# Kernel tuning notes

Measured on AMD Instinct MI355X. Metric: run time of the kernel, lower is better.

The kernel has to match this reference:

```python
import jax, jax.numpy as jnp
import numpy as np

H = 1024

def _gru_layer(x_seq, W_ih, W_hh, b_ih, b_hh):
    # x_seq: [B, T, in]; W_ih: [3H, in]; W_hh: [3H, H]
    B = x_seq.shape[0]
    gx = jnp.einsum('bti,gi->btg', x_seq, W_ih) + b_ih  # [B, T, 3H] input gates precomputed

    def step(h, gx_t):
        gh = h @ W_hh.T + b_hh  # [B, 3H]
        xr, xz, xn = jnp.split(gx_t, 3, axis=-1)
        hr, hz, hn = jnp.split(gh, 3, axis=-1)
        r = jax.nn.sigmoid(xr + hr)
        z = jax.nn.sigmoid(xz + hz)
        n = jnp.tanh(xn + r * hn)
        h_new = (1.0 - z) * n + z * h
        return h_new, h_new

    h0 = jnp.zeros((B, W_hh.shape[1]), dtype=x_seq.dtype)
    _, out = jax.lax.scan(step, h0, jnp.swapaxes(gx, 0, 1))  # scan over T
    return jnp.swapaxes(out, 0, 1)  # [B, T, H]

def setup_inputs() -> dict:
    key = jax.random.key(0)
    ks = jax.random.split(key, 8)
    s = 0.03  # ~1/sqrt(H) init scale to avoid gate saturation
    return {
        'tokens': jax.random.randint(ks[0], (16, 1024), 0, 32000),
        'emb': jax.random.normal(ks[1], (32000, H), jnp.float32),
        'W_ih_l0': jax.random.normal(ks[2], (3 * H, H), jnp.float32) * s,
        'W_hh_l0': jax.random.normal(ks[3], (3 * H, H), jnp.float32) * s,
        'b_ih_l0': jnp.zeros((3 * H,), jnp.float32),
        'b_hh_l0': jnp.zeros((3 * H,), jnp.float32),
        'W_ih_l1': jax.random.normal(ks[4], (3 * H, H), jnp.float32) * s,
        'W_hh_l1': jax.random.normal(ks[5], (3 * H, H), jnp.float32) * s,
        'b_ih_l1': jnp.zeros((3 * H,), jnp.float32),
        'b_hh_l1': jnp.zeros((3 * H,), jnp.float32),
        'W_lin': jax.random.normal(ks[6], (128, H), jnp.float32) * s,
        'b_lin': jnp.zeros((128,), jnp.float32),
    }

def reference(tokens, emb, W_ih_l0, W_hh_l0, b_ih_l0, b_hh_l0,
              W_ih_l1, W_hh_l1, b_ih_l1, b_hh_l1, W_lin, b_lin):
    x = emb[tokens]  # [B, T, H]
    h1 = _gru_layer(x, W_ih_l0, W_hh_l0, b_ih_l0, b_hh_l0)
    h2 = _gru_layer(h1, W_ih_l1, W_hh_l1, b_ih_l1, b_hh_l1)
    logits = jnp.einsum('bth,ch->btc', h2, W_lin) + b_lin  # [B, T, C]
    # F.log_softmax with no dim on a 3D tensor uses dim=1 (PyTorch deprecated default)
    return jax.nn.log_softmax(logits, axis=1)
```

## Files before the change

kernel.cpp:

```cpp
#include <hip/hip_runtime.h>
#include <stdint.h>

typedef unsigned short u16;
typedef __attribute__((ext_vector_type(8))) short short8;
typedef __attribute__((ext_vector_type(4))) float f32x4;

#define T_SEQ 1024
#define HDIM  1024
#define NG    3072
#define SLOT  16384
#define FSTRIDE 32

__device__ __forceinline__ u16 f2bf(float f) {
  unsigned u = __float_as_uint(f);
  u += 0x7FFF + ((u >> 16) & 1);
  return (u16)(u >> 16);
}
__device__ __forceinline__ float bf2f(u16 h) {
  return __uint_as_float(((unsigned)h) << 16);
}

__device__ __forceinline__ void gld16(void* lds, const void* g) {
  __builtin_amdgcn_global_load_lds(
      (const __attribute__((address_space(1))) unsigned*)g,
      (__attribute__((address_space(3))) unsigned*)lds, 16, 0, 0);
}

__device__ __forceinline__ void st_agent_u32(unsigned* p, unsigned v) {
  __hip_atomic_store(p, v, __ATOMIC_RELAXED, __HIP_MEMORY_SCOPE_AGENT);
}
__device__ __forceinline__ unsigned ld_agent_u32(const unsigned* p) {
  return __hip_atomic_load(p, __ATOMIC_RELAXED, __HIP_MEMORY_SCOPE_AGENT);
}

__device__ __forceinline__ void poll16(const unsigned* flags, int wave, int lane, unsigned need) {
  if (lane < 16) {
    const unsigned* f = flags + (size_t)(16 * wave + lane) * FSTRIDE;
    while (ld_agent_u32(f) < need) {}
  }
  asm volatile("" ::: "memory");
}

__global__ void cast5_kernel(const float* __restrict__ s0, const float* __restrict__ s1,
                             const float* __restrict__ s2, const float* __restrict__ s3,
                             const float* __restrict__ s4,
                             u16* __restrict__ d0, u16* __restrict__ d1,
                             u16* __restrict__ d2, u16* __restrict__ d3,
                             u16* __restrict__ d4, unsigned* __restrict__ flags) {
  if (blockIdx.x == 0) {
#pragma unroll
    for (int k = 0; k < 32; ++k) flags[threadIdx.x * 32 + k] = 0;
  }
  int bid = blockIdx.x;
  const float* s; u16* d; size_t base;
  if (bid < 3072)       { s = s0; d = d0; base = (size_t)bid * 1024; }
  else if (bid < 6144)  { s = s1; d = d1; base = (size_t)(bid - 3072) * 1024; }
  else if (bid < 9216)  { s = s2; d = d2; base = (size_t)(bid - 6144) * 1024; }
  else if (bid < 12288) { s = s3; d = d3; base = (size_t)(bid - 9216) * 1024; }
  else                  { s = s4; d = d4; base = (size_t)(bid - 12288) * 1024; }
  size_t i = base + (size_t)threadIdx.x * 4;
  float4 v = *(const float4*)(s + i);
  unsigned lo = (unsigned)f2bf(v.x) | ((unsigned)f2bf(v.y) << 16);
  unsigned hi = (unsigned)f2bf(v.z) | ((unsigned)f2bf(v.w) << 16);
  uint2 o; o.x = lo; o.y = hi;
  *(uint2*)(d + i) = o;
}

__global__ void gather_cast_kernel(const int* __restrict__ tokens,
                                   const float* __restrict__ emb,
                                   u16* __restrict__ xbf) {
  int row = blockIdx.x;
  int tok = tokens[row];
  const float4* src = (const float4*)(emb + (size_t)tok * HDIM);
  float4 v = src[threadIdx.x];
  unsigned lo = (unsigned)f2bf(v.x) | ((unsigned)f2bf(v.y) << 16);
  unsigned hi = (unsigned)f2bf(v.z) | ((unsigned)f2bf(v.w) << 16);
  uint2 o; o.x = lo; o.y = hi;
  *(uint2*)(xbf + (size_t)row * HDIM + (size_t)threadIdx.x * 4) = o;
}

template <bool OUT_BF16, bool A_PACKED, bool ADD_BIAS>
__global__ __launch_bounds__(256)
void gemm_bt(const u16* __restrict__ A, const u16* __restrict__ Bt,
             void* __restrict__ Cout, const float* __restrict__ bias,
             int M, int N) {
  const int K = 1024;
  __shared__ u16 As[128 * 32];
  __shared__ u16 Bs[128 * 32];
  const int tid = threadIdx.x;
  const int wave = tid >> 6, lane = tid & 63;
  const int quad = lane >> 4, l16 = lane & 15;
  const int wm = (wave & 1) * 64, wn = (wave >> 1) * 64;
  const int m0 = blockIdx.x * 128, n0 = blockIdx.y * 128;
  const int srow = tid >> 2, scol = (tid & 3) * 8;

  size_t abase0, abase1;
  {
    int r0 = m0 + srow, r1 = m0 + 64 + srow;
    if (A_PACKED) {
      abase0 = (size_t)((r0 & 1023) + 1) * SLOT + (size_t)(r0 >> 10) * 16 +
               (size_t)(scol & 8) + (size_t)(scol >> 4) * 256;
      abase1 = (size_t)((r1 & 1023) + 1) * SLOT + (size_t)(r1 >> 10) * 16 +
               (size_t)(scol & 8) + (size_t)(scol >> 4) * 256;
    } else {
      abase0 = (size_t)r0 * K + scol;
      abase1 = (size_t)r1 * K + scol;
    }
  }
  const size_t bbase0 = (size_t)(n0 + srow) * K + scol;
  const size_t bbase1 = (size_t)(n0 + 64 + srow) * K + scol;

  f32x4 acc[4][4] = {};

  for (int kk = 0; kk < K; kk += 32) {
    __syncthreads();
    size_t ka = A_PACKED ? (size_t)kk * 16 : (size_t)kk;
    gld16(&As[srow * 32 + scol],        A + abase0 + ka);
    gld16(&As[(64 + srow) * 32 + scol], A + abase1 + ka);
    gld16(&Bs[srow * 32 + scol],        Bt + bbase0 + kk);
    gld16(&Bs[(64 + srow) * 32 + scol], Bt + bbase1 + kk);
    __syncthreads();
    short8 af[4], bfr[4];
#pragma unroll
    for (int mt = 0; mt < 4; ++mt)
      af[mt] = *(const short8*)&As[(wm + mt * 16 + l16) * 32 + quad * 8];
#pragma unroll
    for (int nt = 0; nt < 4; ++nt)
      bfr[nt] = *(const short8*)&Bs[(wn + nt * 16 + l16) * 32 + quad * 8];
#pragma unroll
    for (int mt = 0; mt < 4; ++mt)
#pragma unroll
      for (int nt = 0; nt < 4; ++nt)
        acc[mt][nt] = __builtin_amdgcn_mfma_f32_16x16x32_bf16(af[mt], bfr[nt], acc[mt][nt], 0, 0, 0);
  }
#pragma unroll
  for (int mt = 0; mt < 4; ++mt) {
#pragma unroll
    for (int nt = 0; nt < 4; ++nt) {
#pragma unroll
      for (int r = 0; r < 4; ++r) {
        int m = m0 + wm + mt * 16 + quad * 4 + r;
        int n = n0 + wn + nt * 16 + l16;
        float v = acc[mt][nt][r];
        if (ADD_BIAS) v += bias[n];
        if (OUT_BF16) ((u16*)Cout)[(size_t)m * N + n] = f2bf(v);
        else          ((float*)Cout)[(size_t)m * N + n] = v;
      }
    }
  }
}

__global__ __launch_bounds__(256, 1)
void fused_scan_kernel(const u16* __restrict__ gx0,
                       u16* __restrict__ h1p, u16* __restrict__ h2p,
                       const u16* __restrict__ Whh0, const u16* __restrict__ Wih1,
                       const u16* __restrict__ Whh1,
                       const float* __restrict__ bih0, const float* __restrict__ bhh0,
                       const float* __restrict__ bih1, const float* __restrict__ bhh1,
                       unsigned* __restrict__ flags0, unsigned* __restrict__ flags1) {
  const int tid = threadIdx.x;
  const int wave = tid >> 6, lane = tid & 63;
  const int quad = lane >> 4, l16 = lane & 15;
  const int eb = tid >> 4, ej = tid & 15;

  __shared__ float part[4][6][256];
  __shared__ float biasS[2][3][16];

  const int fragoff = (16 * wave + (quad >> 1)) * 256 + l16 * 16 + (quad & 1) * 8;

  if (blockIdx.x < 64) {
    const int wg = blockIdx.x, j0 = wg * 16;
    short8 wf[3][8];
#pragma unroll
    for (int g = 0; g < 3; ++g)
#pragma unroll
      for (int s = 0; s < 8; ++s)
        wf[g][s] = *(const short8*)&Whh0[(size_t)(g * 1024 + j0 + l16) * 1024 + wave * 256 + s * 32 + quad * 8];
    if (tid < 96) {
      int a = tid / 48, rem = tid % 48, g = rem >> 4, jl = rem & 15;
      biasS[a][g][jl] = (a ? bhh0 : bih0)[g * 1024 + j0 + jl];
    }
    if (tid < 128) st_agent_u32((unsigned*)h1p + wg * 128 + tid, 0u);
    __syncthreads();
    if (tid == 0)
      __hip_atomic_store(flags0 + (size_t)wg * FSTRIDE, 1u, __ATOMIC_RELEASE, __HIP_MEMORY_SCOPE_AGENT);

    const u16* gxp = gx0 + (size_t)eb * T_SEQ * NG + j0 + ej;
    u16 gxu0 = gxp[0], gxu1 = gxp[1024], gxu2 = gxp[2048];
    float hprev = 0.f;

    for (int t = 0; t < T_SEQ; ++t) {
      poll16(flags0, wave, lane, (unsigned)(t + 1));
      int tn = (t + 1 < T_SEQ) ? t + 1 : t;
      const u16* gpn = gx0 + ((size_t)eb * T_SEQ + tn) * NG + j0 + ej;
      u16 ng0 = gpn[0], ng1 = gpn[1024], ng2 = gpn[2048];
      const u16* src = h1p + (size_t)t * SLOT + fragoff;
      short8 af[8];
#pragma unroll
      for (int s = 0; s < 8; ++s) af[s] = *(const short8*)(src + s * 512);
      f32x4 a0 = {0.f,0.f,0.f,0.f}, a1 = {0.f,0.f,0.f,0.f}, a2 = {0.f,0.f,0.f,0.f};
#pragma unroll
      for (int s = 0; s < 8; ++s) {
        a0 = __builtin_amdgcn_mfma_f32_16x16x32_bf16(af[s], wf[0][s], a0, 0, 0, 0);
        a1 = __builtin_amdgcn_mfma_f32_16x16x32_bf16(af[s], wf[1][s], a1, 0, 0, 0);
        a2 = __builtin_amdgcn_mfma_f32_16x16x32_bf16(af[s], wf[2][s], a2, 0, 0, 0);
      }
#pragma unroll
      for (int r = 0; r < 4; ++r) {
        int o = (quad * 4 + r) * 16 + l16;
        part[wave][0][o] = a0[r]; part[wave][1][o] = a1[r]; part[wave][2][o] = a2[r];
      }
      __syncthreads();
      float ghr = part[0][0][tid] + part[1][0][tid] + part[2][0][tid] + part[3][0][tid] + biasS[1][0][ej];
      float ghz = part[0][1][tid] + part[1][1][tid] + part[2][1][tid] + part[3][1][tid] + biasS[1][1][ej];
      float ghn = part[0][2][tid] + part[1][2][tid] + part[2][2][tid] + part[3][2][tid] + biasS[1][2][ej];
      float xr = bf2f(gxu0) + biasS[0][0][ej] + ghr;
      float xz = bf2f(gxu1) + biasS[0][1][ej] + ghz;
      float xn = bf2f(gxu2) + biasS[0][2][ej];
      float r_ = 1.f / (1.f + __expf(-xr));
      float z_ = 1.f / (1.f + __expf(-xz));
      float pre = fminf(fmaxf(xn + r_ * ghn, -15.f), 15.f);
      float e2 = __expf(2.f * pre);
      float n_ = (e2 - 1.f) / (e2 + 1.f);
      float hn = (1.f - z_) * n_ + z_ * hprev;
      hprev = hn;
      gxu0 = ng0; gxu1 = ng1; gxu2 = ng2;

      unsigned mine = (unsigned)f2bf(hn);
      unsigned other = __shfl_xor(mine, 1);
      if (!(tid & 1))
        st_agent_u32((unsigned*)h1p + (size_t)(t + 1) * (SLOT / 2) + wg * 128 + (tid >> 1),
                     mine | (other << 16));
      __syncthreads();
      if (tid == 0)
        __hip_atomic_store(flags0 + (size_t)wg * FSTRIDE, (unsigned)(t + 2), __ATOMIC_RELEASE, __HIP_MEMORY_SCOPE_AGENT);
    }
  } else {
    const int wg = blockIdx.x - 64, j0 = wg * 16;
    short8 wfX[3][8], wfH[3][8];
#pragma unroll
    for (int g = 0; g < 3; ++g)
#pragma unroll
      for (int s = 0; s < 8; ++s) {
        size_t row = (size_t)(g * 1024 + j0 + l16) * 1024 + wave * 256 + s * 32 + quad * 8;
        wfX[g][s] = *(const short8*)&Wih1[row];
        wfH[g][s] = *(const short8*)&Whh1[row];
      }
    if (tid < 96) {
      int a = tid / 48, rem = tid % 48, g = rem >> 4, jl = rem & 15;
      biasS[a][g][jl] = (a ? bhh1 : bih1)[g * 1024 + j0 + jl];
    }
    if (tid < 128) st_agent_u32((unsigned*)h2p + wg * 128 + tid, 0u);
    __syncthreads();
    if (tid == 0)
      __hip_atomic_store(flags1 + (size_t)wg * FSTRIDE, 1u, __ATOMIC_RELEASE, __HIP_MEMORY_SCOPE_AGENT);

    short8 af1[8];
    poll16(flags0, wave, lane, 2u);
    {
      const u16* s1 = h1p + (size_t)SLOT + fragoff;
#pragma unroll
      for (int s = 0; s < 8; ++s) af1[s] = *(const short8*)(s1 + s * 512);
    }
    float hprev = 0.f;

    for (int t = 0; t < T_SEQ; ++t) {
      f32x4 x0 = {0.f,0.f,0.f,0.f}, x1 = {0.f,0.f,0.f,0.f}, x2 = {0.f,0.f,0.f,0.f};
#pragma unroll
      for (int s = 0; s < 8; ++s) {
        x0 = __builtin_amdgcn_mfma_f32_16x16x32_bf16(af1[s], wfX[0][s], x0, 0, 0, 0);
        x1 = __builtin_amdgcn_mfma_f32_16x16x32_bf16(af1[s], wfX[1][s], x1, 0, 0, 0);
        x2 = __builtin_amdgcn_mfma_f32_16x16x32_bf16(af1[s], wfX[2][s], x2, 0, 0, 0);
      }
      poll16(flags1, wave, lane, (unsigned)(t + 1));
      short8 af2[8];
      const u16* s2 = h2p + (size_t)t * SLOT + fragoff;
#pragma unroll
      for (int s = 0; s < 8; ++s) af2[s] = *(const short8*)(s2 + s * 512);
      if (t + 1 < T_SEQ) {
        poll16(flags0, wave, lane, (unsigned)(t + 3));
        const u16* s1 = h1p + (size_t)(t + 2) * SLOT + fragoff;
#pragma unroll
        for (int s = 0; s < 8; ++s) af1[s] = *(const short8*)(s1 + s * 512);
      }
      f32x4 h0 = {0.f,0.f,0.f,0.f}, h1a = {0.f,0.f,0.f,0.f}, h2a = {0.f,0.f,0.f,0.f};
#pragma unroll
      for (int s = 0; s < 8; ++s) {
        h0  = __builtin_amdgcn_mfma_f32_16x16x32_bf16(af2[s], wfH[0][s], h0, 0, 0, 0);
        h1a = __builtin_amdgcn_mfma_f32_16x16x32_bf16(af2[s], wfH[1][s], h1a, 0, 0, 0);
        h2a = __builtin_amdgcn_mfma_f32_16x16x32_bf16(af2[s], wfH[2][s], h2a, 0, 0, 0);
      }
#pragma unroll
      for (int r = 0; r < 4; ++r) {
        int o = (quad * 4 + r) * 16 + l16;
        part[wave][0][o] = x0[r];  part[wave][1][o] = x1[r];  part[wave][2][o] = x2[r];
        part[wave][3][o] = h0[r];  part[wave][4][o] = h1a[r]; part[wave][5][o] = h2a[r];
      }
      __syncthreads();
      float sxr = part[0][0][tid] + part[1][0][tid] + part[2][0][tid] + part[3][0][tid] + biasS[0][0][ej];
      float sxz = part[0][1][tid] + part[1][1][tid] + part[2][1][tid] + part[3][1][tid] + biasS[0][1][ej];
      float sxn = part[0][2][tid] + part[1][2][tid] + part[2][2][tid] + part[3][2][tid] + biasS[0][2][ej];
      float shr = part[0][3][tid] + part[1][3][tid] + part[2][3][tid] + part[3][3][tid] + biasS[1][0][ej];
      float shz = part[0][4][tid] + part[1][4][tid] + part[2][4][tid] + part[3][4][tid] + biasS[1][1][ej];
      float shn = part[0][5][tid] + part[1][5][tid] + part[2][5][tid] + part[3][5][tid] + biasS[1][2][ej];
      float r_ = 1.f / (1.f + __expf(-(sxr + shr)));
      float z_ = 1.f / (1.f + __expf(-(sxz + shz)));
      float pre = fminf(fmaxf(sxn + r_ * shn, -15.f), 15.f);
      float e2 = __expf(2.f * pre);
      float n_ = (e2 - 1.f) / (e2 + 1.f);
      float hn = (1.f - z_) * n_ + z_ * hprev;
      hprev = hn;

      unsigned mine = (unsigned)f2bf(hn);
      unsigned other = __shfl_xor(mine, 1);
      if (!(tid & 1))
        st_agent_u32((unsigned*)h2p + (size_t)(t + 1) * (SLOT / 2) + wg * 128 + (tid >> 1),
                     mine | (other << 16));
      __syncthreads();
      if (tid == 0)
        __hip_atomic_store(flags1 + (size_t)wg * FSTRIDE, (unsigned)(t + 2), __ATOMIC_RELEASE, __HIP_MEMORY_SCOPE_AGENT);
    }
  }
}

__global__ void logsoftmax_kernel(float* __restrict__ out) {
  int b = blockIdx.x, cg = blockIdx.y;
  int ci = threadIdx.x & 15, ts = threadIdx.x >> 4;
  int c = cg * 16 + ci;
  float m = -1e30f, s = 0.f;
  for (int t = ts; t < T_SEQ; t += 16) {
    float v = out[((size_t)b * T_SEQ + t) * 128 + c];
    if (v > m) { s = s * __expf(m - v) + 1.f; m = v; }
    else s += __expf(v - m);
  }
  __shared__ float mS[16][16], sS[16][16];
  mS[ts][ci] = m; sS[ts][ci] = s;
  __syncthreads();
  if (ts == 0) {
    float M = mS[0][ci], S = sS[0][ci];
#pragma unroll
    for (int k = 1; k < 16; ++k) {
      float m2 = mS[k][ci], s2 = sS[k][ci];
      float nm = fmaxf(M, m2);
      S = S * __expf(M - nm) + s2 * __expf(m2 - nm);
      M = nm;
    }
    sS[0][ci] = M + logf(S);
  }
  __syncthreads();
  float lsd = sS[0][ci];
  for (int t = ts; t < T_SEQ; t += 16) {
    size_t i = ((size_t)b * T_SEQ + t) * 128 + c;
    out[i] -= lsd;
  }
}

extern "C" void kernel_launch(void* const* d_in, const int* in_sizes, int n_in,
                              void* d_out, int out_size, void* d_ws, size_t ws_size,
                              hipStream_t stream) {
  const int*   tokens = (const int*)d_in[0];
  const float* emb  = (const float*)d_in[1];
  const float* Wih0 = (const float*)d_in[2];
  const float* Whh0 = (const float*)d_in[3];
  const float* bih0 = (const float*)d_in[4];
  const float* bhh0 = (const float*)d_in[5];
  const float* Wih1 = (const float*)d_in[6];
  const float* Whh1 = (const float*)d_in[7];
  const float* bih1 = (const float*)d_in[8];
  const float* bhh1 = (const float*)d_in[9];
  const float* Wlin = (const float*)d_in[10];
  const float* blin = (const float*)d_in[11];
  float* out = (float*)d_out;

  uint8_t* ws = (uint8_t*)d_ws;
  size_t off = 0;
  auto alloc = [&](size_t bytes) -> void* {
    void* p = ws + off;
    off += (bytes + 255) & ~(size_t)255;
    return p;
  };
  u16* h1p   = (u16*)alloc((size_t)(T_SEQ + 1) * SLOT * 2);
  u16* h2p   = (u16*)alloc((size_t)(T_SEQ + 1) * SLOT * 2);
  u16* xbf   = h2p;
  u16* gxbuf = (u16*)alloc((size_t)16384 * NG * 2);
  u16* wih0b = (u16*)alloc((size_t)NG * HDIM * 2);
  u16* whh0b = (u16*)alloc((size_t)NG * HDIM * 2);
  u16* wih1b = (u16*)alloc((size_t)NG * HDIM * 2);
  u16* whh1b = (u16*)alloc((size_t)NG * HDIM * 2);
  u16* wlinb = (u16*)alloc((size_t)128 * HDIM * 2);
  unsigned* flags = (unsigned*)alloc(32768);

  cast5_kernel<<<dim3(12416), dim3(256), 0, stream>>>(
      Wih0, Whh0, Wih1, Whh1, Wlin, wih0b, whh0b, wih1b, whh1b, wlinb, flags);
  gather_cast_kernel<<<dim3(16384), dim3(256), 0, stream>>>(tokens, emb, xbf);
  gemm_bt<true, false, false><<<dim3(128, 24), dim3(256), 0, stream>>>(
      xbf, wih0b, gxbuf, nullptr, 16384, NG);
  fused_scan_kernel<<<dim3(128), dim3(256), 0, stream>>>(
      gxbuf, h1p, h2p, whh0b, wih1b, whh1b, bih0, bhh0, bih1, bhh1,
      flags, flags + 64 * FSTRIDE);
  gemm_bt<false, true, true><<<dim3(128, 1), dim3(256), 0, stream>>>(
      h2p, wlinb, out, blin, 16384, 128);
  logsoftmax_kernel<<<dim3(16, 8), dim3(256), 0, stream>>>(out);
}
```

Before: 3.883 ms.

## Replace flag polling with tagged-data handoff and ring buffer in GRU scan

Each hidden-state word is now stored as a 64-bit pair of two bf16 values plus a step tag, so consumers poll the data itself instead of a separate per-workgroup release flag. This removes the flag store, release fence and barrier from each step. Layer 0 writes into a 64-slot ring buffer and only occasionally waits on layer-1 progress counters, and layer 1's input weights move from registers to LDS. The cost is double the bytes per hidden-state transfer, a clear kernel over a larger workspace, and a reworked A-operand load in the final projection GEMM to unpack the tagged layout.

Measured after the change: 6.340 ms. 1.63x slower.

```diff
diff --git a/kernel.cpp b/kernel.cpp
--- a/kernel.cpp
+++ b/kernel.cpp
@@ -2,13 +2,16 @@
 #include <stdint.h>
 
 typedef unsigned short u16;
+typedef unsigned int u32;
+typedef unsigned long long u64;
 typedef __attribute__((ext_vector_type(8))) short short8;
 typedef __attribute__((ext_vector_type(4))) float f32x4;
 
 #define T_SEQ 1024
 #define HDIM  1024
 #define NG    3072
-#define SLOT  16384
+#define RING  64
+#define SLOTU 16384
 #define FSTRIDE 32
 
 __device__ __forceinline__ u16 f2bf(float f) {
@@ -33,12 +36,36 @@
   return __hip_atomic_load(p, __ATOMIC_RELAXED, __HIP_MEMORY_SCOPE_AGENT);
 }
 
-__device__ __forceinline__ void poll16(const unsigned* flags, int wave, int lane, unsigned need) {
-  if (lane < 16) {
-    const unsigned* f = flags + (size_t)(16 * wave + lane) * FSTRIDE;
-    while (ld_agent_u32(f) < need) {}
-  }
-  asm volatile("" ::: "memory");
+__device__ __forceinline__ void load_slot(short8 af[8], const u64* slot64,
+                                          int fb64, unsigned exptag) {
+  for (;;) {
+    unsigned bad = 0;
+#pragma unroll
+    for (int s = 0; s < 8; ++s) {
+      const u64* p = slot64 + fb64 + s * 256;
+      u64 w0 = __hip_atomic_load(p + 0, __ATOMIC_RELAXED, __HIP_MEMORY_SCOPE_AGENT);
+      u64 w1 = __hip_atomic_load(p + 1, __ATOMIC_RELAXED, __HIP_MEMORY_SCOPE_AGENT);
+      u64 w2 = __hip_atomic_load(p + 2, __ATOMIC_RELAXED, __HIP_MEMORY_SCOPE_AGENT);
+      u64 w3 = __hip_atomic_load(p + 3, __ATOMIC_RELAXED, __HIP_MEMORY_SCOPE_AGENT);
+      bad |= ((unsigned)(w0 >> 32) ^ exptag) | ((unsigned)(w1 >> 32) ^ exptag) |
+             ((unsigned)(w2 >> 32) ^ exptag) | ((unsigned)(w3 >> 32) ^ exptag);
+      uint4 q; q.x = (unsigned)w0; q.y = (unsigned)w1; q.z = (unsigned)w2; q.w = (unsigned)w3;
+      af[s] = *(const short8*)&q;
+    }
+    if (__ballot(bad == 0) == ~0ull) return;
+  }
+}
+
+__device__ __forceinline__ void store_pair(unsigned* base32, size_t idx32,
+                                           unsigned pk, unsigned tag) {
+  u64 w = (u64)pk | ((u64)tag << 32);
+  __hip_atomic_store((u64*)base32 + (idx32 >> 1), w,
+                     __ATOMIC_RELAXED, __HIP_MEMORY_SCOPE_AGENT);
+}
+
+__global__ void clear_kernel(uint4* __restrict__ p, unsigned n) {
+  unsigned i = blockIdx.x * 256 + threadIdx.x;
+  if (i < n) { uint4 z; z.x = z.y = z.z = z.w = 0u; p[i] = z; }
 }
 
 __global__ void cast5_kernel(const float* __restrict__ s0, const float* __restrict__ s1,
@@ -46,11 +73,7 @@
                              const float* __restrict__ s4,
                              u16* __restrict__ d0, u16* __restrict__ d1,
                              u16* __restrict__ d2, u16* __restrict__ d3,
-                             u16* __restrict__ d4, unsigned* __restrict__ flags) {
-  if (blockIdx.x == 0) {
-#pragma unroll
-    for (int k = 0; k < 32; ++k) flags[threadIdx.x * 32 + k] = 0;
-  }
+                             u16* __restrict__ d4) {
   int bid = blockIdx.x;
   const float* s; u16* d; size_t base;
   if (bid < 3072)       { s = s0; d = d0; base = (size_t)bid * 1024; }
@@ -79,13 +102,13 @@
   *(uint2*)(xbf + (size_t)row * HDIM + (size_t)threadIdx.x * 4) = o;
 }
 
-template <bool OUT_BF16, bool A_PACKED, bool ADD_BIAS>
+template <bool OUT_BF16, int AMODE, bool ADD_BIAS>
 __global__ __launch_bounds__(256)
 void gemm_bt(const u16* __restrict__ A, const u16* __restrict__ Bt,
              void* __restrict__ Cout, const float* __restrict__ bias,
              int M, int N) {
   const int K = 1024;
-  __shared__ u16 As[128 * 32];
+  __shared__ __align__(16) unsigned char AsRaw[16384];
   __shared__ u16 Bs[128 * 32];
   const int tid = threadIdx.x;
   const int wave = tid >> 6, lane = tid & 63;
@@ -94,18 +117,20 @@
   const int m0 = blockIdx.x * 128, n0 = blockIdx.y * 128;
   const int srow = tid >> 2, scol = (tid & 3) * 8;
 
-  size_t abase0, abase1;
-  {
-    int r0 = m0 + srow, r1 = m0 + 64 + srow;
-    if (A_PACKED) {
-      abase0 = (size_t)((r0 & 1023) + 1) * SLOT + (size_t)(r0 >> 10) * 16 +
-               (size_t)(scol & 8) + (size_t)(scol >> 4) * 256;
-      abase1 = (size_t)((r1 & 1023) + 1) * SLOT + (size_t)(r1 >> 10) * 16 +
-               (size_t)(scol & 8) + (size_t)(scol >> 4) * 256;
-    } else {
-      abase0 = (size_t)r0 * K + scol;
-      abase1 = (size_t)r1 * K + scol;
-    }
+  size_t abase0 = 0, abase1 = 0;
+  size_t abaseP[4];
+  if constexpr (AMODE == 1) {
+    int li = tid & 7;
+#pragma unroll
+    for (int rd = 0; rd < 4; ++rd) {
+      int r = m0 + rd * 32 + (tid >> 3);
+      int b = r >> 10, tt = r & 1023;
+      abaseP[rd] = (size_t)(tt + 1) * SLOTU + (size_t)b * 16 +
+                   (size_t)(li >> 2) * 256 + (size_t)(li & 3) * 4;
+    }
+  } else {
+    abase0 = (size_t)(m0 + srow) * K + scol;
+    abase1 = (size_t)(m0 + 64 + srow) * K + scol;
   }
   const size_t bbase0 = (size_t)(n0 + srow) * K + scol;
   const size_t bbase1 = (size_t)(n0 + 64 + srow) * K + scol;
@@ -114,16 +139,37 @@
 
   for (int kk = 0; kk < K; kk += 32) {
     __syncthreads();
-    size_t ka = A_PACKED ? (size_t)kk * 16 : (size_t)kk;
-    gld16(&As[srow * 32 + scol],        A + abase0 + ka);
-    gld16(&As[(64 + srow) * 32 + scol], A + abase1 + ka);
+    if constexpr (AMODE == 1) {
+      u32* As32 = (u32*)AsRaw;
+      const u32* Apk = (const u32*)A;
+#pragma unroll
+      for (int rd = 0; rd < 4; ++rd)
+        gld16(As32 + rd * 1024 + tid * 4, Apk + abaseP[rd] + (size_t)(kk >> 4) * 256);
+    } else {
+      u16* As = (u16*)AsRaw;
+      gld16(&As[srow * 32 + scol],        A + abase0 + kk);
+      gld16(&As[(64 + srow) * 32 + scol], A + abase1 + kk);
+    }
     gld16(&Bs[srow * 32 + scol],        Bt + bbase0 + kk);
     gld16(&Bs[(64 + srow) * 32 + scol], Bt + bbase1 + kk);
     __syncthreads();
     short8 af[4], bfr[4];
-#pragma unroll
-    for (int mt = 0; mt < 4; ++mt)
-      af[mt] = *(const short8*)&As[(wm + mt * 16 + l16) * 32 + quad * 8];
+    if constexpr (AMODE == 1) {
+      const u32* As32 = (const u32*)AsRaw;
+#pragma unroll
+      for (int mt = 0; mt < 4; ++mt) {
+        const uint4* q = (const uint4*)&As32[(wm + mt * 16 + l16) * 32 +
+                                             (quad >> 1) * 16 + (quad & 1) * 8];
+        uint4 q0 = q[0], q1 = q[1];
+        uint4 d; d.x = q0.x; d.y = q0.z; d.z = q1.x; d.w = q1.z;
+        af[mt] = *(const short8*)&d;
+      }
+    } else {
+      const u16* As = (const u16*)AsRaw;
+#pragma unroll
+      for (int mt = 0; mt < 4; ++mt)
+        af[mt] = *(const short8*)&As[(wm + mt * 16 + l16) * 32 + quad * 8];
+    }
 #pragma unroll
     for (int nt = 0; nt < 4; ++nt)
       bfr[nt] = *(const short8*)&Bs[(wn + nt * 16 + l16) * 32 + quad * 8];
@@ -152,12 +198,12 @@
 
 __global__ __launch_bounds__(256, 1)
 void fused_scan_kernel(const u16* __restrict__ gx0,
-                       u16* __restrict__ h1p, u16* __restrict__ h2p,
+                       unsigned* __restrict__ h1p, unsigned* __restrict__ h2p,
                        const u16* __restrict__ Whh0, const u16* __restrict__ Wih1,
                        const u16* __restrict__ Whh1,
                        const float* __restrict__ bih0, const float* __restrict__ bhh0,
                        const float* __restrict__ bih1, const float* __restrict__ bhh1,
-                       unsigned* __restrict__ flags0, unsigned* __restrict__ flags1) {
+                       unsigned* __restrict__ prog) {
   const int tid = threadIdx.x;
   const int wave = tid >> 6, lane = tid & 63;
   const int quad = lane >> 4, l16 = lane & 15;
@@ -165,8 +211,9 @@
 
   __shared__ float part[4][6][256];
   __shared__ float biasS[2][3][16];
-
-  const int fragoff = (16 * wave + (quad >> 1)) * 256 + l16 * 16 + (quad & 1) * 8;
+  __shared__ u16 wx[4 * 3 * 8 * 4 * 16 * 8];
+
+  const int fb64 = (((16 * wave + (quad >> 1)) * 256 + l16 * 16 + (quad & 1) * 8) >> 1);
 
   if (blockIdx.x < 64) {
     const int wg = blockIdx.x, j0 = wg * 16;
@@ -180,24 +227,19 @@
       int a = tid / 48, rem = tid % 48, g = rem >> 4, jl = rem & 15;
       biasS[a][g][jl] = (a ? bhh0 : bih0)[g * 1024 + j0 + jl];
     }
-    if (tid < 128) st_agent_u32((unsigned*)h1p + wg * 128 + tid, 0u);
-    __syncthreads();
-    if (tid == 0)
-      __hip_atomic_store(flags0 + (size_t)wg * FSTRIDE, 1u, __ATOMIC_RELEASE, __HIP_MEMORY_SCOPE_AGENT);
-
     const u16* gxp = gx0 + (size_t)eb * T_SEQ * NG + j0 + ej;
     u16 gxu0 = gxp[0], gxu1 = gxp[1024], gxu2 = gxp[2048];
     float hprev = 0.f;
+    unsigned vfgen = 64;
 
     for (int t = 0; t < T_SEQ; ++t) {
-      poll16(flags0, wave, lane, (unsigned)(t + 1));
       int tn = (t + 1 < T_SEQ) ? t + 1 : t;
       const u16* gpn = gx0 + ((size_t)eb * T_SEQ + tn) * NG + j0 + ej;
       u16 ng0 = gpn[0], ng1 = gpn[1024], ng2 = gpn[2048];
-      const u16* src = h1p + (size_t)t * SLOT + fragoff;
+
       short8 af[8];
-#pragma unroll
-      for (int s = 0; s < 8; ++s) af[s] = *(const short8*)(src + s * 512);
+      load_slot(af, (const u64*)h1p + (size_t)(t & (RING - 1)) * (SLOTU / 2), fb64, (unsigned)t);
+
       f32x4 a0 = {0.f,0.f,0.f,0.f}, a1 = {0.f,0.f,0.f,0.f}, a2 = {0.f,0.f,0.f,0.f};
 #pragma unroll
       for (int s = 0; s < 8; ++s) {
@@ -226,63 +268,60 @@
       hprev = hn;
       gxu0 = ng0; gxu1 = ng1; gxu2 = ng2;
 
+      if ((unsigned)(t + 1) > vfgen) {
+        unsigned thr = (unsigned)(t - 32);
+        for (;;) {
+          unsigned v = 0xFFFFFFFFu;
+          if (lane < 16) v = ld_agent_u32(prog + (size_t)(16 * wave + lane) * FSTRIDE);
+          if (__ballot(v >= thr) == ~0ull) break;
+        }
+        vfgen = thr + 65;
+      }
+
       unsigned mine = (unsigned)f2bf(hn);
       unsigned other = __shfl_xor(mine, 1);
       if (!(tid & 1))
-        st_agent_u32((unsigned*)h1p + (size_t)(t + 1) * (SLOT / 2) + wg * 128 + (tid >> 1),
-                     mine | (other << 16));
+        store_pair(h1p, (size_t)((t + 1) & (RING - 1)) * SLOTU + wg * 256 + eb * 16 + ej,
+                   mine | (other << 16), (unsigned)(t + 1));
       __syncthreads();
-      if (tid == 0)
-        __hip_atomic_store(flags0 + (size_t)wg * FSTRIDE, (unsigned)(t + 2), __ATOMIC_RELEASE, __HIP_MEMORY_SCOPE_AGENT);
     }
   } else {
     const int wg = blockIdx.x - 64, j0 = wg * 16;
-    short8 wfX[3][8], wfH[3][8];
+    short8 wfH[3][8];
 #pragma unroll
     for (int g = 0; g < 3; ++g)
 #pragma unroll
       for (int s = 0; s < 8; ++s) {
         size_t row = (size_t)(g * 1024 + j0 + l16) * 1024 + wave * 256 + s * 32 + quad * 8;
-        wfX[g][s] = *(const short8*)&Wih1[row];
         wfH[g][s] = *(const short8*)&Whh1[row];
+        short8 wv = *(const short8*)&Wih1[row];
+        *(short8*)&wx[((((wave * 3 + g) * 8 + s) * 4 + quad) * 16 + l16) * 8] = wv;
       }
     if (tid < 96) {
       int a = tid / 48, rem = tid % 48, g = rem >> 4, jl = rem & 15;
       biasS[a][g][jl] = (a ? bhh1 : bih1)[g * 1024 + j0 + jl];
     }
-    if (tid < 128) st_agent_u32((unsigned*)h2p + wg * 128 + tid, 0u);
-    __syncthreads();
-    if (tid == 0)
-      __hip_atomic_store(flags1 + (size_t)wg * FSTRIDE, 1u, __ATOMIC_RELEASE, __HIP_MEMORY_SCOPE_AGENT);
-
+    float hprev = 0.f;
     short8 af1[8];
-    poll16(flags0, wave, lane, 2u);
-    {
-      const u16* s1 = h1p + (size_t)SLOT + fragoff;
-#pragma unroll
-      for (int s = 0; s < 8; ++s) af1[s] = *(const short8*)(s1 + s * 512);
-    }
-    float hprev = 0.f;
+    load_slot(af1, (const u64*)h1p + (size_t)1 * (SLOTU / 2), fb64, 1u);
 
     for (int t = 0; t < T_SEQ; ++t) {
       f32x4 x0 = {0.f,0.f,0.f,0.f}, x1 = {0.f,0.f,0.f,0.f}, x2 = {0.f,0.f,0.f,0.f};
 #pragma unroll
       for (int s = 0; s < 8; ++s) {
-        x0 = __builtin_amdgcn_mfma_f32_16x16x32_bf16(af1[s], wfX[0][s], x0, 0, 0, 0);
-        x1 = __builtin_amdgcn_mfma_f32_16x16x32_bf16(af1[s], wfX[1][s], x1, 0, 0, 0);
-        x2 = __builtin_amdgcn_mfma_f32_16x16x32_bf16(af1[s], wfX[2][s], x2, 0, 0, 0);
-      }
-      poll16(flags1, wave, lane, (unsigned)(t + 1));
+        short8 w0 = *(const short8*)&wx[((((wave * 3 + 0) * 8 + s) * 4 + quad) * 16 + l16) * 8];
+        short8 w1 = *(const short8*)&wx[((((wave * 3 + 1) * 8 + s) * 4 + quad) * 16 + l16) * 8];
+        short8 w2 = *(const short8*)&wx[((((wave * 3 + 2) * 8 + s) * 4 + quad) * 16 + l16) * 8];
+        x0 = __builtin_amdgcn_mfma_f32_16x16x32_bf16(af1[s], w0, x0, 0, 0, 0);
+        x1 = __builtin_amdgcn_mfma_f32_16x16x32_bf16(af1[s], w1, x1, 0, 0, 0);
+        x2 = __builtin_amdgcn_mfma_f32_16x16x32_bf16(af1[s], w2, x2, 0, 0, 0);
+      }
       short8 af2[8];
-      const u16* s2 = h2p + (size_t)t * SLOT + fragoff;
-#pragma unroll
-      for (int s = 0; s < 8; ++s) af2[s] = *(const short8*)(s2 + s * 512);
-      if (t + 1 < T_SEQ) {
-        poll16(flags0, wave, lane, (unsigned)(t + 3));
-        const u16* s1 = h1p + (size_t)(t + 2) * SLOT + fragoff;
-#pragma unroll
-        for (int s = 0; s < 8; ++s) af1[s] = *(const short8*)(s1 + s * 512);
-      }
+      load_slot(af2, (const u64*)h2p + (size_t)t * (SLOTU / 2), fb64, (unsigned)t);
+      if (t + 1 < T_SEQ)
+        load_slot(af1, (const u64*)h1p + (size_t)((t + 2) & (RING - 1)) * (SLOTU / 2), fb64,
+                  (unsigned)(t + 2));
+
       f32x4 h0 = {0.f,0.f,0.f,0.f}, h1a = {0.f,0.f,0.f,0.f}, h2a = {0.f,0.f,0.f,0.f};
 #pragma unroll
       for (int s = 0; s < 8; ++s) {
@@ -314,11 +353,11 @@
       unsigned mine = (unsigned)f2bf(hn);
       unsigned other = __shfl_xor(mine, 1);
       if (!(tid & 1))
-        st_agent_u32((unsigned*)h2p + (size_t)(t + 1) * (SLOT / 2) + wg * 128 + (tid >> 1),
-                     mine | (other << 16));
+        store_pair(h2p, (size_t)(t + 1) * SLOTU + wg * 256 + eb * 16 + ej,
+                   mine | (other << 16), (unsigned)(t + 1));
       __syncthreads();
       if (tid == 0)
-        __hip_atomic_store(flags1 + (size_t)wg * FSTRIDE, (unsigned)(t + 2), __ATOMIC_RELEASE, __HIP_MEMORY_SCOPE_AGENT);
+        st_agent_u32(prog + (size_t)wg * FSTRIDE, (unsigned)(t + 1));
     }
   }
 }
@@ -379,26 +418,29 @@
     off += (bytes + 255) & ~(size_t)255;
     return p;
   };
-  u16* h1p   = (u16*)alloc((size_t)(T_SEQ + 1) * SLOT * 2);
-  u16* h2p   = (u16*)alloc((size_t)(T_SEQ + 1) * SLOT * 2);
-  u16* xbf   = h2p;
+  unsigned* h1p  = (unsigned*)alloc((size_t)RING * SLOTU * 4);
+  unsigned* h2p  = (unsigned*)alloc((size_t)(T_SEQ + 1) * SLOTU * 4);
+  unsigned* prog = (unsigned*)alloc((size_t)64 * FSTRIDE * 4);
+  size_t clearBytes = (size_t)RING * SLOTU * 4 + (size_t)(T_SEQ + 1) * SLOTU * 4 +
+                      (size_t)64 * FSTRIDE * 4;
+  u16* xbf   = (u16*)h2p;
   u16* gxbuf = (u16*)alloc((size_t)16384 * NG * 2);
   u16* wih0b = (u16*)alloc((size_t)NG * HDIM * 2);
   u16* whh0b = (u16*)alloc((size_t)NG * HDIM * 2);
   u16* wih1b = (u16*)alloc((size_t)NG * HDIM * 2);
   u16* whh1b = (u16*)alloc((size_t)NG * HDIM * 2);
   u16* wlinb = (u16*)alloc((size_t)128 * HDIM * 2);
-  unsigned* flags = (unsigned*)alloc(32768);
 
   cast5_kernel<<<dim3(12416), dim3(256), 0, stream>>>(
-      Wih0, Whh0, Wih1, Whh1, Wlin, wih0b, whh0b, wih1b, whh1b, wlinb, flags);
+      Wih0, Whh0, Wih1, Whh1, Wlin, wih0b, whh0b, wih1b, whh1b, wlinb);
   gather_cast_kernel<<<dim3(16384), dim3(256), 0, stream>>>(tokens, emb, xbf);
-  gemm_bt<true, false, false><<<dim3(128, 24), dim3(256), 0, stream>>>(
+  gemm_bt<true, 0, false><<<dim3(128, 24), dim3(256), 0, stream>>>(
       xbf, wih0b, gxbuf, nullptr, 16384, NG);
+  unsigned n16 = (unsigned)(clearBytes / 16);
+  clear_kernel<<<dim3((n16 + 255) / 256), dim3(256), 0, stream>>>((uint4*)h1p, n16);
   fused_scan_kernel<<<dim3(128), dim3(256), 0, stream>>>(
-      gxbuf, h1p, h2p, whh0b, wih1b, whh1b, bih0, bhh0, bih1, bhh1,
-      flags, flags + 64 * FSTRIDE);
-  gemm_bt<false, true, true><<<dim3(128, 1), dim3(256), 0, stream>>>(
-      h2p, wlinb, out, blin, 16384, 128);
+      gxbuf, h1p, h2p, whh0b, wih1b, whh1b, bih0, bhh0, bih1, bhh1, prog);
+  gemm_bt<false, 1, true><<<dim3(128, 1), dim3(256), 0, stream>>>(
+      (const u16*)h2p, wlinb, out, blin, 16384, 128);
   logsoftmax_kernel<<<dim3(16, 8), dim3(256), 0, stream>>>(out);
 }
```

## Use per-wave flags, double-buffered partials, LDS-resident Wih1, and timestep-major gx layout

Applied to the files above, without the earlier changes.

The scan kernel now publishes progress per wave instead of per block. Each wave waits for its own stores to complete and sets its own flag, which removes the two block-wide barriers per step, and consumers poll 64 flags per wave. The partial-sum LDS buffer is double-buffered so the single remaining barrier per step is enough. The layer-1 Wih1 fragments move from registers to LDS to relieve register pressure, and the gx GEMM writes its output in a timestep-major layout so each step reads gx contiguously. The risks are more polling traffic across 64 lanes, extra LDS reads per step, and flag ordering that relies on s_waitcnt instead of release atomics.

Result: faster. 3.263 ms (-16.0%).

```diff
diff --git a/kernel.cpp b/kernel.cpp
--- a/kernel.cpp
+++ b/kernel.cpp
@@ -2,6 +2,7 @@
 #include <stdint.h>
 
 typedef unsigned short u16;
+typedef unsigned int u32;
 typedef __attribute__((ext_vector_type(8))) short short8;
 typedef __attribute__((ext_vector_type(4))) float f32x4;
 
@@ -33,11 +34,9 @@
   return __hip_atomic_load(p, __ATOMIC_RELAXED, __HIP_MEMORY_SCOPE_AGENT);
 }
 
-__device__ __forceinline__ void poll16(const unsigned* flags, int wave, int lane, unsigned need) {
-  if (lane < 16) {
-    const unsigned* f = flags + (size_t)(16 * wave + lane) * FSTRIDE;
-    while (ld_agent_u32(f) < need) {}
-  }
+__device__ __forceinline__ void poll64(const unsigned* flags, int wave, int lane, unsigned need) {
+  const unsigned* f = flags + (size_t)(64 * wave + lane) * FSTRIDE;
+  while (ld_agent_u32(f) < need) {}
   asm volatile("" ::: "memory");
 }
 
@@ -49,7 +48,7 @@
                              u16* __restrict__ d4, unsigned* __restrict__ flags) {
   if (blockIdx.x == 0) {
 #pragma unroll
-    for (int k = 0; k < 32; ++k) flags[threadIdx.x * 32 + k] = 0;
+    for (int k = 0; k < 64; ++k) flags[threadIdx.x * 64 + k] = 0;
   }
   int bid = blockIdx.x;
   const float* s; u16* d; size_t base;
@@ -79,7 +78,7 @@
   *(uint2*)(xbf + (size_t)row * HDIM + (size_t)threadIdx.x * 4) = o;
 }
 
-template <bool OUT_BF16, bool A_PACKED, bool ADD_BIAS>
+template <int OUT_MODE, bool A_PACKED, bool ADD_BIAS>
 __global__ __launch_bounds__(256)
 void gemm_bt(const u16* __restrict__ A, const u16* __restrict__ Bt,
              void* __restrict__ Cout, const float* __restrict__ bias,
@@ -143,8 +142,13 @@
         int n = n0 + wn + nt * 16 + l16;
         float v = acc[mt][nt][r];
         if (ADD_BIAS) v += bias[n];
-        if (OUT_BF16) ((u16*)Cout)[(size_t)m * N + n] = f2bf(v);
-        else          ((float*)Cout)[(size_t)m * N + n] = v;
+        if (OUT_MODE == 2) {
+          int t = m & 1023, b = m >> 10, g = n >> 10, c = n & 1023;
+          size_t idx = ((((size_t)t * 64 + (c >> 4)) * 3 + g) * 16 + b) * 16 + (c & 15);
+          ((u16*)Cout)[idx] = f2bf(v);
+        } else {
+          ((float*)Cout)[(size_t)m * N + n] = v;
+        }
       }
     }
   }
@@ -152,7 +156,7 @@
 
 __global__ __launch_bounds__(256, 1)
 void fused_scan_kernel(const u16* __restrict__ gx0,
-                       u16* __restrict__ h1p, u16* __restrict__ h2p,
+                       u16* __restrict__ h1seq, u16* __restrict__ h2seq,
                        const u16* __restrict__ Whh0, const u16* __restrict__ Wih1,
                        const u16* __restrict__ Whh1,
                        const float* __restrict__ bih0, const float* __restrict__ bhh0,
@@ -163,8 +167,9 @@
   const int quad = lane >> 4, l16 = lane & 15;
   const int eb = tid >> 4, ej = tid & 15;
 
-  __shared__ float part[4][6][256];
+  __shared__ float part[2][4][6][256];
   __shared__ float biasS[2][3][16];
+  __shared__ u16 wx[4 * 3 * 8 * 4 * 16 * 8];
 
   const int fragoff = (16 * wave + (quad >> 1)) * 256 + l16 * 16 + (quad & 1) * 8;
 
@@ -180,21 +185,18 @@
       int a = tid / 48, rem = tid % 48, g = rem >> 4, jl = rem & 15;
       biasS[a][g][jl] = (a ? bhh0 : bih0)[g * 1024 + j0 + jl];
     }
-    if (tid < 128) st_agent_u32((unsigned*)h1p + wg * 128 + tid, 0u);
-    __syncthreads();
-    if (tid == 0)
-      __hip_atomic_store(flags0 + (size_t)wg * FSTRIDE, 1u, __ATOMIC_RELEASE, __HIP_MEMORY_SCOPE_AGENT);
-
-    const u16* gxp = gx0 + (size_t)eb * T_SEQ * NG + j0 + ej;
-    u16 gxu0 = gxp[0], gxu1 = gxp[1024], gxu2 = gxp[2048];
+    if (lane < 32) st_agent_u32((unsigned*)h1seq + wg * 128 + wave * 32 + lane, 0u);
+    asm volatile("s_waitcnt vmcnt(0)" ::: "memory");
+    if (lane == 0) st_agent_u32(flags0 + (size_t)(wg * 4 + wave) * FSTRIDE, 1u);
+
+    const u16* gxp = gx0 + (size_t)(wg * 3) * 256 + eb * 16 + ej;
+    u16 gxu0 = gxp[0], gxu1 = gxp[256], gxu2 = gxp[512];
     float hprev = 0.f;
 
     for (int t = 0; t < T_SEQ; ++t) {
-      poll16(flags0, wave, lane, (unsigned)(t + 1));
-      int tn = (t + 1 < T_SEQ) ? t + 1 : t;
-      const u16* gpn = gx0 + ((size_t)eb * T_SEQ + tn) * NG + j0 + ej;
-      u16 ng0 = gpn[0], ng1 = gpn[1024], ng2 = gpn[2048];
-      const u16* src = h1p + (size_t)t * SLOT + fragoff;
+      const int pb = t & 1;
+      poll64(flags0, wave, lane, (unsigned)(t + 1));
+      const u16* src = h1seq + (size_t)t * SLOT + fragoff;
       short8 af[8];
 #pragma unroll
       for (int s = 0; s < 8; ++s) af[s] = *(const short8*)(src + s * 512);
@@ -208,12 +210,12 @@
 #pragma unroll
       for (int r = 0; r < 4; ++r) {
         int o = (quad * 4 + r) * 16 + l16;
-        part[wave][0][o] = a0[r]; part[wave][1][o] = a1[r]; part[wave][2][o] = a2[r];
+        part[pb][wave][0][o] = a0[r]; part[pb][wave][1][o] = a1[r]; part[pb][wave][2][o] = a2[r];
       }
       __syncthreads();
-      float ghr = part[0][0][tid] + part[1][0][tid] + part[2][0][tid] + part[3][0][tid] + biasS[1][0][ej];
-      float ghz = part[0][1][tid] + part[1][1][tid] + part[2][1][tid] + part[3][1][tid] + biasS[1][1][ej];
-      float ghn = part[0][2][tid] + part[1][2][tid] + part[2][2][tid] + part[3][2][tid] + biasS[1][2][ej];
+      float ghr = part[pb][0][0][tid] + part[pb][1][0][tid] + part[pb][2][0][tid] + part[pb][3][0][tid] + biasS[1][0][ej];
+      float ghz = part[pb][0][1][tid] + part[pb][1][1][tid] + part[pb][2][1][tid] + part[pb][3][1][tid] + biasS[1][1][ej];
+      float ghn = part[pb][0][2][tid] + part[pb][1][2][tid] + part[pb][2][2][tid] + part[pb][3][2][tid] + biasS[1][2][ej];
       float xr = bf2f(gxu0) + biasS[0][0][ej] + ghr;
       float xz = bf2f(gxu1) + biasS[0][1][ej] + ghz;
       float xn = bf2f(gxu2) + biasS[0][2][ej];
@@ -224,62 +226,68 @@
       float n_ = (e2 - 1.f) / (e2 + 1.f);
       float hn = (1.f - z_) * n_ + z_ * hprev;
       hprev = hn;
-      gxu0 = ng0; gxu1 = ng1; gxu2 = ng2;
 
       unsigned mine = (unsigned)f2bf(hn);
       unsigned other = __shfl_xor(mine, 1);
       if (!(tid & 1))
-        st_agent_u32((unsigned*)h1p + (size_t)(t + 1) * (SLOT / 2) + wg * 128 + (tid >> 1),
+        st_agent_u32((unsigned*)h1seq + (size_t)(t + 1) * (SLOT / 2) + wg * 128 + (tid >> 1),
                      mine | (other << 16));
-      __syncthreads();
-      if (tid == 0)
-        __hip_atomic_store(flags0 + (size_t)wg * FSTRIDE, (unsigned)(t + 2), __ATOMIC_RELEASE, __HIP_MEMORY_SCOPE_AGENT);
+      asm volatile("s_waitcnt vmcnt(0)" ::: "memory");
+      if (lane == 0)
+        st_agent_u32(flags0 + (size_t)(wg * 4 + wave) * FSTRIDE, (unsigned)(t + 2));
+      int tn = (t + 1 < T_SEQ) ? t + 1 : t;
+      const u16* gpn = gx0 + (size_t)(tn * 64 + wg) * 3 * 256 + eb * 16 + ej;
+      gxu0 = gpn[0]; gxu1 = gpn[256]; gxu2 = gpn[512];
     }
   } else {
     const int wg = blockIdx.x - 64, j0 = wg * 16;
-    short8 wfX[3][8], wfH[3][8];
+    short8 wfH[3][8];
 #pragma unroll
     for (int g = 0; g < 3; ++g)
 #pragma unroll
       for (int s = 0; s < 8; ++s) {
         size_t row = (size_t)(g * 1024 + j0 + l16) * 1024 + wave * 256 + s * 32 + quad * 8;
-        wfX[g][s] = *(const short8*)&Wih1[row];
         wfH[g][s] = *(const short8*)&Whh1[row];
+        short8 wv = *(const short8*)&Wih1[row];
+        *(short8*)&wx[((((wave * 3 + g) * 8 + s) * 4 + quad) * 16 + l16) * 8] = wv;
       }
     if (tid < 96) {
       int a = tid / 48, rem = tid % 48, g = rem >> 4, jl = rem & 15;
       biasS[a][g][jl] = (a ? bhh1 : bih1)[g * 1024 + j0 + jl];
     }
-    if (tid < 128) st_agent_u32((unsigned*)h2p + wg * 128 + tid, 0u);
-    __syncthreads();
-    if (tid == 0)
-      __hip_atomic_store(flags1 + (size_t)wg * FSTRIDE, 1u, __ATOMIC_RELEASE, __HIP_MEMORY_SCOPE_AGENT);
-
+    if (lane < 32) st_agent_u32((unsigned*)h2seq + wg * 128 + wave * 32 + lane, 0u);
+    asm volatile("s_waitcnt vmcnt(0)" ::: "memory");
+    if (lane == 0) st_agent_u32(flags1 + (size_t)(wg * 4 + wave) * FSTRIDE, 1u);
+
+    float hprev = 0.f;
     short8 af1[8];
-    poll16(flags0, wave, lane, 2u);
+    poll64(flags0, wave, lane, 2u);
     {
-      const u16* s1 = h1p + (size_t)SLOT + fragoff;
+      const u16* s1 = h1seq + (size_t)SLOT + fragoff;
 #pragma unroll
       for (int s = 0; s < 8; ++s) af1[s] = *(const short8*)(s1 + s * 512);
     }
-    float hprev = 0.f;
 
     for (int t = 0; t < T_SEQ; ++t) {
+      const int pb = t & 1;
       f32x4 x0 = {0.f,0.f,0.f,0.f}, x1 = {0.f,0.f,0.f,0.f}, x2 = {0.f,0.f,0.f,0.f};
 #pragma unroll
       for (int s = 0; s < 8; ++s) {
-        x0 = __builtin_amdgcn_mfma_f32_16x16x32_bf16(af1[s], wfX[0][s], x0, 0, 0, 0);
-        x1 = __builtin_amdgcn_mfma_f32_16x16x32_bf16(af1[s], wfX[1][s], x1, 0, 0, 0);
-        x2 = __builtin_amdgcn_mfma_f32_16x16x32_bf16(af1[s], wfX[2][s], x2, 0, 0, 0);
-      }
-      poll16(flags1, wave, lane, (unsigned)(t + 1));
+        short8 w0 = *(const short8*)&wx[((((wave * 3 + 0) * 8 + s) * 4 + quad) * 16 + l16) * 8];
+        short8 w1 = *(const short8*)&wx[((((wave * 3 + 1) * 8 + s) * 4 + quad) * 16 + l16) * 8];
+        short8 w2 = *(const short8*)&wx[((((wave * 3 + 2) * 8 + s) * 4 + quad) * 16 + l16) * 8];
+        x0 = __builtin_amdgcn_mfma_f32_16x16x32_bf16(af1[s], w0, x0, 0, 0, 0);
+        x1 = __builtin_amdgcn_mfma_f32_16x16x32_bf16(af1[s], w1, x1, 0, 0, 0);
+        x2 = __builtin_amdgcn_mfma_f32_16x16x32_bf16(af1[s], w2, x2, 0, 0, 0);
+      }
+      poll64(flags1, wave, lane, (unsigned)(t + 1));
       short8 af2[8];
-      const u16* s2 = h2p + (size_t)t * SLOT + fragoff;
+      const u16* s2 = h2seq + (size_t)t * SLOT + fragoff;
 #pragma unroll
       for (int s = 0; s < 8; ++s) af2[s] = *(const short8*)(s2 + s * 512);
       if (t + 1 < T_SEQ) {
-        poll16(flags0, wave, lane, (unsigned)(t + 3));
-        const u16* s1 = h1p + (size_t)(t + 2) * SLOT + fragoff;
+        poll64(flags0, wave, lane, (unsigned)(t + 3));
+        const u16* s1 = h1seq + (size_t)(t + 2) * SLOT + fragoff;
 #pragma unroll
         for (int s = 0; s < 8; ++s) af1[s] = *(const short8*)(s1 + s * 512);
       }
@@ -293,16 +301,16 @@
 #pragma unroll
       for (int r = 0; r < 4; ++r) {
         int o = (quad * 4 + r) * 16 + l16;
-        part[wave][0][o] = x0[r];  part[wave][1][o] = x1[r];  part[wave][2][o] = x2[r];
-        part[wave][3][o] = h0[r];  part[wave][4][o] = h1a[r]; part[wave][5][o] = h2a[r];
+        part[pb][wave][0][o] = x0[r];  part[pb][wave][1][o] = x1[r];  part[pb][wave][2][o] = x2[r];
+        part[pb][wave][3][o] = h0[r];  part[pb][wave][4][o] = h1a[r]; part[pb][wave][5][o] = h2a[r];
       }
       __syncthreads();
-      float sxr = part[0][0][tid] + part[1][0][tid] + part[2][0][tid] + part[3][0][tid] + biasS[0][0][ej];
-      float sxz = part[0][1][tid] + part[1][1][tid] + part[2][1][tid] + part[3][1][tid] + biasS[0][1][ej];
-      float sxn = part[0][2][tid] + part[1][2][tid] + part[2][2][tid] + part[3][2][tid] + biasS[0][2][ej];
-      float shr = part[0][3][tid] + part[1][3][tid] + part[2][3][tid] + part[3][3][tid] + biasS[1][0][ej];
-      float shz = part[0][4][tid] + part[1][4][tid] + part[2][4][tid] + part[3][4][tid] + biasS[1][1][ej];
-      float shn = part[0][5][tid] + part[1][5][tid] + part[2][5][tid] + part[3][5][tid] + biasS[1][2][ej];
+      float sxr = part[pb][0][0][tid] + part[pb][1][0][tid] + part[pb][2][0][tid] + part[pb][3][0][tid] + biasS[0][0][ej];
+      float sxz = part[pb][0][1][tid] + part[pb][1][1][tid] + part[pb][2][1][tid] + part[pb][3][1][tid] + biasS[0][1][ej];
+      float sxn = part[pb][0][2][tid] + part[pb][1][2][tid] + part[pb][2][2][tid] + part[pb][3][2][tid] + biasS[0][2][ej];
+      float shr = part[pb][0][3][tid] + part[pb][1][3][tid] + part[pb][2][3][tid] + part[pb][3][3][tid] + biasS[1][0][ej];
+      float shz = part[pb][0][4][tid] + part[pb][1][4][tid] + part[pb][2][4][tid] + part[pb][3][4][tid] + biasS[1][1][ej];
+      float shn = part[pb][0][5][tid] + part[pb][1][5][tid] + part[pb][2][5][tid] + part[pb][3][5][tid] + biasS[1][2][ej];
       float r_ = 1.f / (1.f + __expf(-(sxr + shr)));
       float z_ = 1.f / (1.f + __expf(-(sxz + shz)));
       float pre = fminf(fmaxf(sxn + r_ * shn, -15.f), 15.f);
@@ -314,11 +322,11 @@
       unsigned mine = (unsigned)f2bf(hn);
       unsigned other = __shfl_xor(mine, 1);
       if (!(tid & 1))
-        st_agent_u32((unsigned*)h2p + (size_t)(t + 1) * (SLOT / 2) + wg * 128 + (tid >> 1),
+        st_agent_u32((unsigned*)h2seq + (size_t)(t + 1) * (SLOT / 2) + wg * 128 + (tid >> 1),
                      mine | (other << 16));
-      __syncthreads();
-      if (tid == 0)
-        __hip_atomic_store(flags1 + (size_t)wg * FSTRIDE, (unsigned)(t + 2), __ATOMIC_RELEASE, __HIP_MEMORY_SCOPE_AGENT);
+      asm volatile("s_waitcnt vmcnt(0)" ::: "memory");
+      if (lane == 0)
+        st_agent_u32(flags1 + (size_t)(wg * 4 + wave) * FSTRIDE, (unsigned)(t + 2));
     }
   }
 }
@@ -379,26 +387,25 @@
     off += (bytes + 255) & ~(size_t)255;
     return p;
   };
-  u16* h1p   = (u16*)alloc((size_t)(T_SEQ + 1) * SLOT * 2);
-  u16* h2p   = (u16*)alloc((size_t)(T_SEQ + 1) * SLOT * 2);
-  u16* xbf   = h2p;
+  u16* h1seq = (u16*)alloc((size_t)(T_SEQ + 1) * SLOT * 2);
+  u16* h2seq = (u16*)alloc((size_t)(T_SEQ + 1) * SLOT * 2);
   u16* gxbuf = (u16*)alloc((size_t)16384 * NG * 2);
   u16* wih0b = (u16*)alloc((size_t)NG * HDIM * 2);
   u16* whh0b = (u16*)alloc((size_t)NG * HDIM * 2);
   u16* wih1b = (u16*)alloc((size_t)NG * HDIM * 2);
   u16* whh1b = (u16*)alloc((size_t)NG * HDIM * 2);
   u16* wlinb = (u16*)alloc((size_t)128 * HDIM * 2);
-  unsigned* flags = (unsigned*)alloc(32768);
+  unsigned* flags = (unsigned*)alloc(65536);
 
   cast5_kernel<<<dim3(12416), dim3(256), 0, stream>>>(
       Wih0, Whh0, Wih1, Whh1, Wlin, wih0b, whh0b, wih1b, whh1b, wlinb, flags);
-  gather_cast_kernel<<<dim3(16384), dim3(256), 0, stream>>>(tokens, emb, xbf);
-  gemm_bt<true, false, false><<<dim3(128, 24), dim3(256), 0, stream>>>(
-      xbf, wih0b, gxbuf, nullptr, 16384, NG);
+  gather_cast_kernel<<<dim3(16384), dim3(256), 0, stream>>>(tokens, emb, h1seq);
+  gemm_bt<2, false, false><<<dim3(128, 24), dim3(256), 0, stream>>>(
+      h1seq, wih0b, gxbuf, nullptr, 16384, NG);
   fused_scan_kernel<<<dim3(128), dim3(256), 0, stream>>>(
-      gxbuf, h1p, h2p, whh0b, wih1b, whh1b, bih0, bhh0, bih1, bhh1,
-      flags, flags + 64 * FSTRIDE);
-  gemm_bt<false, true, true><<<dim3(128, 1), dim3(256), 0, stream>>>(
-      h2p, wlinb, out, blin, 16384, 128);
+      gxbuf, h1seq, h2seq, whh0b, wih1b, whh1b, bih0, bhh0, bih1, bhh1,
+      flags, flags + 256 * FSTRIDE);
+  gemm_bt<0, true, true><<<dim3(128, 1), dim3(256), 0, stream>>>(
+      h2seq, wlinb, out, blin, 16384, 128);
   logsoftmax_kernel<<<dim3(16, 8), dim3(256), 0, stream>>>(out);
 }
```
